# Kernel tuning notes

Measured on AMD Instinct MI355X. Metric: run time of the kernel, lower is better.

The kernel has to match this reference:

```python
import jax, jax.numpy as jnp
import numpy as np

B, S, D, H = 8, 1024, 768, 12
C = D // H  # head dim = 64
NEG_SLOPE = 0.2  # PyG GATConv default leaky_relu slope


def setup_inputs() -> dict:
    key = jax.random.key(0)
    ks = jax.random.split(key, 12)
    s = 0.02
    return {
        "hidden_states": jax.random.normal(ks[0], (B, S, D), jnp.float32),
        "transformer_output": jax.random.normal(ks[1], (B, S, D), jnp.float32),
        # GATConv params: lin (no bias), att_src/att_dst [H, C], bias [H*C]
        "W_gat": jax.random.normal(ks[2], (D, D), jnp.float32) * s,
        "att_src": jax.random.normal(ks[3], (H, C), jnp.float32) * s,
        "att_dst": jax.random.normal(ks[4], (H, C), jnp.float32) * s,
        "b_gat": jnp.zeros((D,), jnp.float32),
        # gat_projection
        "W_proj": jax.random.normal(ks[5], (D, D), jnp.float32) * s,
        "b_proj": jnp.zeros((D,), jnp.float32),
        # fusion
        "W_fus": jax.random.normal(ks[6], (2 * D, D), jnp.float32) * s,
        "b_fus": jnp.zeros((D,), jnp.float32),
    }


def reference(hidden_states, transformer_output, W_gat, att_src, att_dst,
              b_gat, W_proj, b_proj, W_fus, b_fus):
    # --- GATConv on a fully-connected graph (+ default self-loops) ---
    # Fully connected + self loops => softmax over ALL sources per target,
    # so the scatter-softmax reduces to dense attention.
    x = (hidden_states @ W_gat).reshape(B, S, H, C)          # [B,S,H,C]
    a_src = jnp.einsum('bshc,hc->bhs', x, att_src)           # score contribution of source j
    a_dst = jnp.einsum('bshc,hc->bhs', x, att_dst)           # score contribution of target i
    # scores[b,h,i,j] = a_dst_i + a_src_j, then leaky_relu, softmax over j
    scores = jax.nn.leaky_relu(a_dst[:, :, :, None] + a_src[:, :, None, :],
                               negative_slope=NEG_SLOPE)     # [B,H,S,S]
    attn = jax.nn.softmax(scores, axis=-1)
    out = jnp.einsum('bhij,bjhc->bihc', attn, x)             # aggregate sources
    gat_out = out.reshape(B, S, D) + b_gat                   # concat heads + bias

    # --- projection, fusion ---
    graph_output = gat_out @ W_proj + b_proj
    fused = jnp.concatenate([transformer_output, graph_output], axis=-1)
    fused = fused @ W_fus + b_fus
    return fused
```

## Files before the change

kernel.cpp:

```cpp
#include <hip/hip_runtime.h>
#include <hip/hip_bf16.h>

#define NB 8
#define NS 1024
#define ND 768
#define NH 12
#define NC 64
#define NEG 0.2f
#define NBUK 128

typedef __attribute__((ext_vector_type(8))) short bf16x8;
typedef __attribute__((ext_vector_type(4))) float f32x4;

static __device__ __forceinline__ float bf2f(unsigned short u) {
    union { float f; unsigned int i; } v; v.i = ((unsigned int)u) << 16; return v.f;
}
static __device__ __forceinline__ unsigned short f2bf(float f) {
    union { float f; unsigned int i; } v; v.f = f;
    unsigned int r = v.i + 0x7FFFu + ((v.i >> 16) & 1u);
    return (unsigned short)(r >> 16);
}

static __device__ __forceinline__ void gload16(const unsigned short* g, unsigned short* l) {
    __builtin_amdgcn_global_load_lds((const __attribute__((address_space(1))) void*)g,
                                     (__attribute__((address_space(3))) void*)l, 16, 0, 0);
}

static __device__ __forceinline__ int swz_bid(int orig, int nwg) {
    int q = nwg >> 3, r = nwg & 7;
    int xcd = orig & 7, idx = orig >> 3;
    return (xcd < r ? xcd * (q + 1) : r * (q + 1) + (xcd - r) * q) + idx;
}

__global__ __launch_bounds__(256) void k_prep(const float* __restrict__ hs, const float* __restrict__ to,
                                              const float* __restrict__ Wp, const float* __restrict__ Wg,
                                              const float* __restrict__ Wf, const float* __restrict__ bp,
                                              const float* __restrict__ bfu,
                                              unsigned short* __restrict__ h_bf, unsigned short* __restrict__ t_bf,
                                              unsigned short* __restrict__ Wp_bf, unsigned short* __restrict__ WgT,
                                              unsigned short* __restrict__ WfT, float* __restrict__ bias_tot,
                                              int n1, int n2) {
    const int NT1 = (ND / 32) * (3 * ND / 32);
    const int NT2 = (ND * 8) / 256;
    int blk = blockIdx.x, t = threadIdx.x;
    if (blk < NT1) {
        __shared__ float tile[32][33];
        int bx = blk % (ND / 32), by = blk / (ND / 32);
        const float* src; unsigned short* dst; int K, k0;
        if (by < ND / 32) { src = Wg; dst = WgT; K = ND; k0 = by * 32; }
        else { src = Wf; dst = WfT; K = 2 * ND; k0 = (by - ND / 32) * 32; }
        int n0 = bx * 32;
        int r = t >> 3, c4 = (t & 7) * 4;
        float4 v = *reinterpret_cast<const float4*>(src + (size_t)(k0 + r) * ND + n0 + c4);
        tile[r][c4] = v.x; tile[r][c4 + 1] = v.y; tile[r][c4 + 2] = v.z; tile[r][c4 + 3] = v.w;
        __syncthreads();
        ushort4 o;
        o.x = f2bf(tile[c4][r]); o.y = f2bf(tile[c4 + 1][r]);
        o.z = f2bf(tile[c4 + 2][r]); o.w = f2bf(tile[c4 + 3][r]);
        *reinterpret_cast<ushort4*>(dst + (size_t)(n0 + r) * K + k0 + c4) = o;
    } else if (blk < NT1 + NT2) {
        int gid = (blk - NT1) * 256 + t;
        int c = gid >> 3, sl = gid & 7;
        float acc = 0.f;
        int k0 = sl * 96;
#pragma unroll 8
        for (int k = k0; k < k0 + 96; k++) acc += bp[k] * Wf[(size_t)(ND + k) * ND + c];
        acc += __shfl_down(acc, 1, 64);
        acc += __shfl_down(acc, 2, 64);
        acc += __shfl_down(acc, 4, 64);
        if (sl == 0) bias_tot[c] = acc + bfu[c];
    } else {
        int gid = (blk - NT1 - NT2) * 256 + t;
        const float* s; unsigned short* d; int i;
        if (gid < n1) { s = hs; d = h_bf; i = gid; }
        else if (gid < 2 * n1) { s = to; d = t_bf; i = gid - n1; }
        else { s = Wp; d = Wp_bf; i = gid - 2 * n1; if (i >= n2) return; }
        i *= 4;
        float4 v = *reinterpret_cast<const float4*>(s + i);
        ushort4 o;
        o.x = f2bf(v.x); o.y = f2bf(v.y); o.z = f2bf(v.z); o.w = f2bf(v.w);
        *reinterpret_cast<ushort4*>(d + i) = o;
    }
}

__global__ __launch_bounds__(256) void k_bsumf(const unsigned short* __restrict__ x_bf,
                                               const float* __restrict__ a_src,
                                               float* __restrict__ P,
                                               float* __restrict__ zb,
                                               float* __restrict__ smax_g,
                                               float2* __restrict__ bparam) {
    int grp = blockIdx.x, bh = blockIdx.y, t = threadIdx.x;
    int b = bh / NH, h = bh % NH;
    __shared__ float v[1024];
    __shared__ float pe1[1024], pe2[1024];
    __shared__ unsigned short pj[1024];
    __shared__ float red[256];
    __shared__ int cnt[NBUK], pre[NBUK], ofs[NBUK], bst[NBUK + 1];
    __shared__ float zs1[NBUK], zs2[NBUK];
    for (int i = t; i < 1024; i += 256) v[i] = a_src[(size_t)bh * 1024 + i];
    if (t < NBUK) { cnt[t] = 0; zs1[t] = 0.f; zs2[t] = 0.f; }
    __syncthreads();
    float lm = -1e30f, ln = 1e30f;
    for (int i = t; i < 1024; i += 256) { lm = fmaxf(lm, v[i]); ln = fminf(ln, v[i]); }
    red[t] = lm; __syncthreads();
    for (int s = 128; s > 0; s >>= 1) { if (t < s) red[t] = fmaxf(red[t], red[t + s]); __syncthreads(); }
    float mx = red[0]; __syncthreads();
    red[t] = ln; __syncthreads();
    for (int s = 128; s > 0; s >>= 1) { if (t < s) red[t] = fminf(red[t], red[t + s]); __syncthreads(); }
    float mn = red[0]; __syncthreads();
    float scale = (float)NBUK / fmaxf(mx - mn, 1e-20f);
    for (int i = t; i < 1024; i += 256) {
        int bk = min(max((int)((v[i] - mn) * scale), 0), NBUK - 1);
        atomicAdd(&cnt[bk], 1);
    }
    __syncthreads();
    if (t < NBUK) pre[t] = cnt[t];
    __syncthreads();
    for (int off = 1; off < NBUK; off <<= 1) {
        int x = (t >= off && t < NBUK) ? pre[t - off] : 0;
        __syncthreads();
        if (t < NBUK) pre[t] += x;
        __syncthreads();
    }
    if (t < NBUK) {
        int start = pre[t] - cnt[t];
        bst[t] = start;
        ofs[t] = start;
    }
    if (t == 0) bst[NBUK] = 1024;
    __syncthreads();
    for (int i = t; i < 1024; i += 256) {
        int bk = min(max((int)((v[i] - mn) * scale), 0), NBUK - 1);
        float u = v[i] - mx;
        float e1 = __expf(u), e2 = __expf(0.2f * u);
        int pos = atomicAdd(&ofs[bk], 1);
        pe1[pos] = e1; pe2[pos] = e2; pj[pos] = (unsigned short)i;
        atomicAdd(&zs1[bk], e1);
        atomicAdd(&zs2[bk], e2);
    }
    __syncthreads();
    for (int off = 1; off < NBUK; off <<= 1) {
        float x1 = (t >= off && t < NBUK) ? zs1[t - off] : 0.f;
        float x2 = (t >= off && t < NBUK) ? zs2[t - off] : 0.f;
        __syncthreads();
        if (t < NBUK) { zs1[t] += x1; zs2[t] += x2; }
        __syncthreads();
    }
    if (grp == 0) {
        if (t < NBUK) {
            zb[(size_t)(bh * NBUK + t) * 2] = zs1[t];
            zb[(size_t)(bh * NBUK + t) * 2 + 1] = zs2[t];
        }
        if (t == 0) { smax_g[bh] = mx; bparam[bh] = make_float2(mn, scale); }
    }
    int w = t >> 6, lane = t & 63;
    const unsigned short* xb = x_bf + (size_t)b * NS * ND + h * 64 + lane;
#pragma unroll
    for (int r = 0; r < 2; r++) {
        int bk = grp * 8 + w * 2 + r;
        int ks = bst[bk], ke = bst[bk + 1];
        float V1 = 0.f, V2 = 0.f;
        for (int k = ks; k < ke; k++) {
            float xv = bf2f(xb[(size_t)pj[k] * ND]);
            V1 += pe1[k] * xv;
            V2 += pe2[k] * xv;
        }
        size_t o = ((size_t)(bh * NBUK + bk) * 2) * 64 + lane;
        P[o] = V1; P[o + 64] = V2;
    }
}

__global__ __launch_bounds__(256) void k_bpref(float* __restrict__ P) {
    int bh = blockIdx.x, t = threadIdx.x, w = t >> 6, lane = t & 63;
    __shared__ float segV[4][2][64];
    size_t base = (size_t)bh * NBUK;
    float V1 = 0.f, V2 = 0.f;
    for (int g = 0; g < 4; ++g) {
        float a1[8], a2[8];
#pragma unroll
        for (int r = 0; r < 8; r++) {
            size_t o = ((base + w * 32 + g * 8 + r) * 2) * 64 + lane;
            a1[r] = P[o]; a2[r] = P[o + 64];
        }
#pragma unroll
        for (int r = 0; r < 8; r++) { V1 += a1[r]; a1[r] = V1; V2 += a2[r]; a2[r] = V2; }
#pragma unroll
        for (int r = 0; r < 8; r++) {
            size_t o = ((base + w * 32 + g * 8 + r) * 2) * 64 + lane;
            P[o] = a1[r]; P[o + 64] = a2[r];
        }
    }
    segV[w][0][lane] = V1; segV[w][1][lane] = V2;
    __syncthreads();
    if (w > 0) {
        float O1 = 0.f, O2 = 0.f;
        for (int w2 = 0; w2 < w; w2++) { O1 += segV[w2][0][lane]; O2 += segV[w2][1][lane]; }
        for (int g = 0; g < 4; ++g) {
            float a1[8], a2[8];
#pragma unroll
            for (int r = 0; r < 8; r++) {
                size_t o = ((base + w * 32 + g * 8 + r) * 2) * 64 + lane;
                a1[r] = P[o]; a2[r] = P[o + 64];
            }
#pragma unroll
            for (int r = 0; r < 8; r++) {
                size_t o = ((base + w * 32 + g * 8 + r) * 2) * 64 + lane;
                P[o] = a1[r] + O1; P[o + 64] = a2[r] + O2;
            }
        }
    }
}

__global__ __launch_bounds__(256) void k_apply3(const float* __restrict__ P,
                                                const float* __restrict__ zb,
                                                const float* __restrict__ a_dst,
                                                const float* __restrict__ smax_g,
                                                const float2* __restrict__ bparam,
                                                const float* __restrict__ b_gat,
                                                unsigned short* __restrict__ gat) {
    int bh = blockIdx.y, t = threadIdx.x, w = t >> 6, lane = t & 63;
    int b = bh / NH, h = bh % NH;
    float sm = smax_g[bh];
    float2 bp_ = bparam[bh];
    float mn = bp_.x, scale = bp_.y;
    size_t pb = (size_t)bh * NBUK;
    float T1 = P[((pb + NBUK - 1) * 2) * 64 + lane];
    float z1tot = zb[(pb + NBUK - 1) * 2];
    float bias = b_gat[h * 64 + lane];
#pragma unroll
    for (int q = 0; q < 8; q++) {
        int i = blockIdx.x * 32 + w * 8 + q;
        float d = a_dst[(size_t)bh * 1024 + i];
        float dm = d + sm;
        float m = dm > 0.f ? dm : NEG * dm;
        float c1 = __expf(dm - m);
        float c2 = __expf(NEG * dm - m);
        int e = (int)floorf((-d - mn) * scale + 0.5f);
        e = min(max(e, 0), NBUK);
        float P1f = 0.f, P2f = 0.f, z1f = 0.f, z2f = 0.f;
        if (e > 0) {
            size_t o = ((pb + e - 1) * 2) * 64 + lane;
            P1f = P[o]; P2f = P[o + 64];
            z1f = zb[(pb + e - 1) * 2];
            z2f = zb[(pb + e - 1) * 2 + 1];
        }
        float num = c1 * (T1 - P1f) + c2 * P2f;
        float Z = c1 * (z1tot - z1f) + c2 * z2f;
        gat[((size_t)(b * NS + i)) * ND + h * 64 + lane] = f2bf(num / Z + bias);
    }
}

template <bool OUT_BF16, bool BIAS, bool DUAL, bool ATT>
static __device__ __forceinline__ void gemm_body(
    const unsigned short* __restrict__ A1, const unsigned short* __restrict__ B1,
    int lda1, int ldb1,
    const unsigned short* __restrict__ A2, const unsigned short* __restrict__ B2,
    int lda2, int ldb2,
    const float* __restrict__ bias, void* __restrict__ Cout,
    int m0, int n0, int N, int K,
    unsigned short* sA, unsigned short* sB,
    const float* __restrict__ att_src, const float* __restrict__ att_dst,
    float* __restrict__ a_src, float* __restrict__ a_dst) {
    int t = threadIdx.x, wave = t >> 6, lane = t & 63;
    int lr = lane & 15, kq = lane >> 4;
    int srow = t >> 3;
    int scol = ((t & 7) ^ (srow & 7)) * 8;
    int cs0 = ((kq) ^ (lr & 7)) * 8;
    int cs1 = ((4 + kq) ^ (lr & 7)) * 8;
    const int kh = K >> 6;
    const int nsteps = (DUAL ? 2 : 1) * kh;
    f32x4 acc[4][2] = {};

    auto STAGE = [&](int s, int buf) {
        const unsigned short* A; const unsigned short* Bt; int lda, ldb, k0;
        if (DUAL && s >= kh) { A = A2; Bt = B2; lda = lda2; ldb = ldb2; k0 = (s - kh) << 6; }
        else { A = A1; Bt = B1; lda = lda1; ldb = ldb1; k0 = s << 6; }
        const unsigned short* gA = A + (size_t)(m0 + srow) * lda + scol + k0;
        const unsigned short* gB = Bt + (size_t)(n0 + srow) * ldb + scol + k0;
        unsigned short* dA = sA + buf * 4096 + t * 8;
        unsigned short* dB = sB + buf * 8192 + t * 8;
        gload16(gA, dA);
        gload16(gA + (size_t)32 * lda, dA + 2048);
        gload16(gB, dB);
        gload16(gB + (size_t)32 * ldb, dB + 2048);
        gload16(gB + (size_t)64 * ldb, dB + 4096);
        gload16(gB + (size_t)96 * ldb, dB + 6144);
    };
    auto COMPUTE = [&](int cur) {
        unsigned short* cA = sA + cur * 4096;
        unsigned short* cB = sB + cur * 8192;
        bf16x8 a0[4], a1v[4], b0[2], b1v[2];
#pragma unroll
        for (int m = 0; m < 4; m++) {
            a0[m]  = *reinterpret_cast<bf16x8*>(&cA[(m * 16 + lr) * 64 + cs0]);
            a1v[m] = *reinterpret_cast<bf16x8*>(&cA[(m * 16 + lr) * 64 + cs1]);
        }
#pragma unroll
        for (int n = 0; n < 2; n++) {
            b0[n]  = *reinterpret_cast<bf16x8*>(&cB[(wave * 32 + n * 16 + lr) * 64 + cs0]);
            b1v[n] = *reinterpret_cast<bf16x8*>(&cB[(wave * 32 + n * 16 + lr) * 64 + cs1]);
        }
#pragma unroll
        for (int m = 0; m < 4; m++)
#pragma unroll
            for (int n = 0; n < 2; n++) {
                acc[m][n] = __builtin_amdgcn_mfma_f32_16x16x32_bf16(a0[m], b0[n], acc[m][n], 0, 0, 0);
                acc[m][n] = __builtin_amdgcn_mfma_f32_16x16x32_bf16(a1v[m], b1v[n], acc[m][n], 0, 0, 0);
            }
    };

    STAGE(0, 0);
    STAGE(1, 1);
    for (int s = 0; s < nsteps - 1; s++) {
        int cur = s & 1;
        asm volatile("s_waitcnt vmcnt(6)" ::: "memory");
        __builtin_amdgcn_s_barrier();
        __builtin_amdgcn_sched_barrier(0);
        COMPUTE(cur);
        __builtin_amdgcn_sched_barrier(0);
        __builtin_amdgcn_s_barrier();
        if (s + 2 < nsteps) STAGE(s + 2, cur);
    }
    asm volatile("s_waitcnt vmcnt(0)" ::: "memory");
    __builtin_amdgcn_s_barrier();
    __builtin_amdgcn_sched_barrier(0);
    COMPUTE((nsteps - 1) & 1);

    int rg = kq * 4;
#pragma unroll
    for (int m = 0; m < 4; m++) {
#pragma unroll
        for (int n = 0; n < 2; n++) {
            int col = n0 + wave * 32 + n * 16 + lr;
            float bv = BIAS ? bias[col] : 0.0f;
#pragma unroll
            for (int r = 0; r < 4; r++) {
                int row = m0 + m * 16 + rg + r;
                float v = acc[m][n][r] + bv;
                if (OUT_BF16) {
                    ((unsigned short*)Cout)[(size_t)row * N + col] = f2bf(v);
                } else {
                    ((float*)Cout)[(size_t)row * N + col] = v;
                }
            }
        }
    }

    if (ATT) {
        __syncthreads();
        float ds_[4][4] = {}, dd_[4][4] = {};
#pragma unroll
        for (int n = 0; n < 2; n++) {
            int colg = n0 + wave * 32 + n * 16 + lr;
            float as_v = att_src[colg];
            float ad_v = att_dst[colg];
#pragma unroll
            for (int m = 0; m < 4; m++)
#pragma unroll
                for (int r = 0; r < 4; r++) {
                    ds_[m][r] = fmaf(acc[m][n][r], as_v, ds_[m][r]);
                    dd_[m][r] = fmaf(acc[m][n][r], ad_v, dd_[m][r]);
                }
        }
#pragma unroll
        for (int off = 1; off <= 8; off <<= 1)
#pragma unroll
            for (int m = 0; m < 4; m++)
#pragma unroll
                for (int r = 0; r < 4; r++) {
                    ds_[m][r] += __shfl_xor(ds_[m][r], off, 64);
                    dd_[m][r] += __shfl_xor(dd_[m][r], off, 64);
                }
        float* red = (float*)sA;
        if (lr == 0) {
#pragma unroll
            for (int m = 0; m < 4; m++)
#pragma unroll
                for (int r = 0; r < 4; r++) {
                    int rl = m * 16 + kq * 4 + r;
                    red[wave * 64 + rl] = ds_[m][r];
                    red[256 + wave * 64 + rl] = dd_[m][r];
                }
        }
        __syncthreads();
        if (t < 128) {
            int hb = t >> 6, rl = t & 63;
            float vs = red[(hb * 2) * 64 + rl] + red[(hb * 2 + 1) * 64 + rl];
            float vd = red[256 + (hb * 2) * 64 + rl] + red[256 + (hb * 2 + 1) * 64 + rl];
            int grow = m0 + rl;
            int b = grow >> 10, sdx = grow & 1023;
            int head = (n0 >> 6) + hb;
            a_src[((size_t)b * NH + head) * NS + sdx] = vs;
            a_dst[((size_t)b * NH + head) * NS + sdx] = vd;
        }
    }
}

__global__ __launch_bounds__(256) void k_gemm_pair(
    const unsigned short* __restrict__ Aa, const unsigned short* __restrict__ Ba,
    unsigned short* __restrict__ Ca, int NBna, int Na, int Ka, int lda_a, int ldb_a, int nwg_a,
    const unsigned short* __restrict__ Ab, const unsigned short* __restrict__ Bb,
    unsigned short* __restrict__ Cb, int NBnb, int Nb, int Kb, int lda_b, int ldb_b,
    const float* __restrict__ att_src, const float* __restrict__ att_dst,
    float* __restrict__ a_src, float* __restrict__ a_dst) {
    __shared__ alignas(16) unsigned short sA[2 * 64 * 64];
    __shared__ alignas(16) unsigned short sB[2 * 128 * 64];
    int wg = swz_bid(blockIdx.x, gridDim.x);
    if (wg < nwg_a) {
        gemm_body<true, false, false, true>(Aa, Ba, lda_a, ldb_a, nullptr, nullptr, 0, 0, nullptr,
                                            Ca, (wg / NBna) * 64, (wg % NBna) * 128, Na, Ka, sA, sB,
                                            att_src, att_dst, a_src, a_dst);
    } else {
        wg -= nwg_a;
        gemm_body<true, false, false, false>(Ab, Bb, lda_b, ldb_b, nullptr, nullptr, 0, 0, nullptr,
                                             Cb, (wg / NBnb) * 64, (wg % NBnb) * 128, Nb, Kb, sA, sB,
                                             nullptr, nullptr, nullptr, nullptr);
    }
}

__global__ __launch_bounds__(256) void k_gemm_dual(
    const unsigned short* __restrict__ A1, const unsigned short* __restrict__ B1,
    const unsigned short* __restrict__ A2, const unsigned short* __restrict__ B2,
    const float* __restrict__ bias, float* __restrict__ out,
    int NBn, int N, int K, int lda, int ldb1, int ldb2) {
    __shared__ alignas(16) unsigned short sA[2 * 64 * 64];
    __shared__ alignas(16) unsigned short sB[2 * 128 * 64];
    int wg = swz_bid(blockIdx.x, gridDim.x);
    gemm_body<false, true, true, false>(A1, B1, lda, ldb1, A2, B2, lda, ldb2, bias,
                                        out, (wg / NBn) * 64, (wg % NBn) * 128, N, K, sA, sB,
                                        nullptr, nullptr, nullptr, nullptr);
}

extern "C" void kernel_launch(void* const* d_in, const int* in_sizes, int n_in,
                              void* d_out, int out_size, void* d_ws, size_t ws_size,
                              hipStream_t stream) {
    const float* hs  = (const float*)d_in[0];
    const float* to  = (const float*)d_in[1];
    const float* Wg  = (const float*)d_in[2];
    const float* asv = (const float*)d_in[3];
    const float* adv = (const float*)d_in[4];
    const float* bg  = (const float*)d_in[5];
    const float* Wp  = (const float*)d_in[6];
    const float* bp  = (const float*)d_in[7];
    const float* Wf  = (const float*)d_in[8];
    const float* bfu = (const float*)d_in[9];
    float* out = (float*)d_out;

    char* ws = (char*)d_ws;
    size_t off = 0;
    auto alloc = [&](size_t bytes) -> void* {
        void* p = ws + off;
        off = (off + bytes + 255) & ~(size_t)255;
        return p;
    };
    const size_t NBSD = (size_t)NB * NS * ND;
    const int NBH = NB * NH;
    unsigned short* h_bf   = (unsigned short*)alloc(NBSD * 2);
    unsigned short* x_bf   = (unsigned short*)alloc(NBSD * 2);
    unsigned short* t_bf   = (unsigned short*)alloc(NBSD * 2);
    unsigned short* WgT    = (unsigned short*)alloc((size_t)ND * ND * 2);
    unsigned short* Wp_bf  = (unsigned short*)alloc((size_t)ND * ND * 2);
    unsigned short* WfT    = (unsigned short*)alloc((size_t)2 * ND * ND * 2);
    unsigned short* WcombT = (unsigned short*)alloc((size_t)ND * ND * 2);
    float*  bias_tot = (float*)alloc((size_t)ND * 4);
    float*  a_src = (float*)alloc((size_t)NBH * NS * 4);
    float*  a_dst = (float*)alloc((size_t)NBH * NS * 4);
    float*  P     = (float*)alloc((size_t)NBH * NBUK * 2 * 64 * 4);
    float*  zb    = (float*)alloc((size_t)NBH * NBUK * 2 * 4);
    float*  smaxb = (float*)alloc((size_t)NBH * 4);
    float2* bparam = (float2*)alloc((size_t)NBH * 8);

    int n1 = (int)NBSD / 4, n2 = ND * ND / 4;
    const int NT1 = (ND / 32) * (3 * ND / 32);
    const int NT2 = (ND * 8) / 256;
    const int NT3 = (2 * n1 + n2 + 255) / 256;
    k_prep<<<NT1 + NT2 + NT3, 256, 0, stream>>>(hs, to, Wp, Wg, Wf, bp, bfu,
                                                h_bf, t_bf, Wp_bf, WgT, WfT, bias_tot, n1, n2);

    int nwg1 = (NB * NS / 64) * (ND / 128);
    int nwgW = (ND / 64) * (ND / 128);
    k_gemm_pair<<<nwg1 + nwgW, 256, 0, stream>>>(
        h_bf, WgT, x_bf, ND / 128, ND, ND, ND, ND, nwg1,
        WfT + ND, Wp_bf, WcombT, ND / 128, ND, ND, 2 * ND, ND,
        asv, adv, a_src, a_dst);

    k_bsumf<<<dim3(NBUK / 8, NBH), 256, 0, stream>>>(x_bf, a_src, P, zb, smaxb, bparam);
    k_bpref<<<NBH, 256, 0, stream>>>(P);

    unsigned short* gat_bf = h_bf;
    k_apply3<<<dim3(NS / 32, NBH), 256, 0, stream>>>(P, zb, a_dst, smaxb, bparam, bg, gat_bf);

    k_gemm_dual<<<(NB * NS / 64) * (ND / 128), 256, 0, stream>>>(
        t_bf, WfT, gat_bf, WcombT, bias_tot, out, ND / 128, ND, ND, ND, 2 * ND, ND);
}
```

Measured before the change: 136.8 us.

## Replace bucket counting-sort with LDS atomic scatter of per-bucket partial sums

The bucket-sum kernel drops the count/prefix/scatter counting sort and its serial per-bucket gather loops. Each block now owns a 16-channel slice of the head and accumulates exp-weighted x values directly into per-bucket LDS arrays with float atomics. The prefix scan of the bucket normalisers moves into k_bpref. This removes the sort barriers and the load imbalance across buckets, but adds heavy LDS atomic contention, which is worst when many sources fall into the same bucket. The grid also shrinks from 16 to 4 blocks per batch-head.

```diff
diff --git a/kernel.cpp b/kernel.cpp
--- a/kernel.cpp
+++ b/kernel.cpp
@@ -83,22 +83,23 @@
     }
 }
 
-__global__ __launch_bounds__(256) void k_bsumf(const unsigned short* __restrict__ x_bf,
-                                               const float* __restrict__ a_src,
-                                               float* __restrict__ P,
-                                               float* __restrict__ zb,
-                                               float* __restrict__ smax_g,
-                                               float2* __restrict__ bparam) {
-    int grp = blockIdx.x, bh = blockIdx.y, t = threadIdx.x;
+__global__ __launch_bounds__(256) void k_psum(const unsigned short* __restrict__ x_bf,
+                                              const float* __restrict__ a_src,
+                                              float* __restrict__ P,
+                                              float* __restrict__ zb,
+                                              float* __restrict__ smax_g,
+                                              float2* __restrict__ bparam) {
+    int cq = blockIdx.x, bh = blockIdx.y, t = threadIdx.x;
     int b = bh / NH, h = bh % NH;
+    int w = t >> 6, lane = t & 63;
+    int c = lane & 15, rr = lane >> 4;
     __shared__ float v[1024];
-    __shared__ float pe1[1024], pe2[1024];
-    __shared__ unsigned short pj[1024];
     __shared__ float red[256];
-    __shared__ int cnt[NBUK], pre[NBUK], ofs[NBUK], bst[NBUK + 1];
-    __shared__ float zs1[NBUK], zs2[NBUK];
+    __shared__ float Pl1[NBUK * 17], Pl2[NBUK * 17];
+    __shared__ float zl1[NBUK], zl2[NBUK];
     for (int i = t; i < 1024; i += 256) v[i] = a_src[(size_t)bh * 1024 + i];
-    if (t < NBUK) { cnt[t] = 0; zs1[t] = 0.f; zs2[t] = 0.f; }
+    for (int i = t; i < NBUK * 17; i += 256) { Pl1[i] = 0.f; Pl2[i] = 0.f; }
+    if (t < NBUK) { zl1[t] = 0.f; zl2[t] = 0.f; }
     __syncthreads();
     float lm = -1e30f, ln = 1e30f;
     for (int i = t; i < 1024; i += 256) { lm = fmaxf(lm, v[i]); ln = fminf(ln, v[i]); }
@@ -109,70 +110,55 @@
     for (int s = 128; s > 0; s >>= 1) { if (t < s) red[t] = fminf(red[t], red[t + s]); __syncthreads(); }
     float mn = red[0]; __syncthreads();
     float scale = (float)NBUK / fmaxf(mx - mn, 1e-20f);
-    for (int i = t; i < 1024; i += 256) {
-        int bk = min(max((int)((v[i] - mn) * scale), 0), NBUK - 1);
-        atomicAdd(&cnt[bk], 1);
+    const unsigned short* xb = x_bf + (size_t)b * NS * ND + h * 64 + cq * 16 + c;
+#pragma unroll 4
+    for (int it = 0; it < 64; it++) {
+        int j = w * 256 + it * 4 + rr;
+        float vj = v[j];
+        int bk = min(max((int)((vj - mn) * scale), 0), NBUK - 1);
+        float u = vj - mx;
+        float e1 = __expf(u), e2 = __expf(0.2f * u);
+        float xv = bf2f(xb[(size_t)j * ND]);
+        atomicAdd(&Pl1[bk * 17 + c], e1 * xv);
+        atomicAdd(&Pl2[bk * 17 + c], e2 * xv);
+        if (cq == 0 && c == 0) { atomicAdd(&zl1[bk], e1); atomicAdd(&zl2[bk], e2); }
     }
     __syncthreads();
-    if (t < NBUK) pre[t] = cnt[t];
+    for (int i = t; i < NBUK * 16; i += 256) {
+        int bk = i >> 4, cc = i & 15;
+        size_t o = ((size_t)(bh * NBUK + bk) * 2) * 64 + cq * 16 + cc;
+        P[o] = Pl1[bk * 17 + cc];
+        P[o + 64] = Pl2[bk * 17 + cc];
+    }
+    if (cq == 0) {
+        if (t < NBUK) {
+            zb[(size_t)(bh * NBUK + t) * 2] = zl1[t];
+            zb[(size_t)(bh * NBUK + t) * 2 + 1] = zl2[t];
+        }
+        if (t == 0) { smax_g[bh] = mx; bparam[bh] = make_float2(mn, scale); }
+    }
+}
+
+__global__ __launch_bounds__(256) void k_bpref(float* __restrict__ P, float* __restrict__ zb) {
+    int bh = blockIdx.x, t = threadIdx.x, w = t >> 6, lane = t & 63;
+    __shared__ float segV[4][2][64];
+    __shared__ float zsh1[NBUK], zsh2[NBUK];
+    if (t < NBUK) {
+        zsh1[t] = zb[(size_t)(bh * NBUK + t) * 2];
+        zsh2[t] = zb[(size_t)(bh * NBUK + t) * 2 + 1];
+    }
     __syncthreads();
     for (int off = 1; off < NBUK; off <<= 1) {
-        int x = (t >= off && t < NBUK) ? pre[t - off] : 0;
+        float x1 = (t >= off && t < NBUK) ? zsh1[t - off] : 0.f;
+        float x2 = (t >= off && t < NBUK) ? zsh2[t - off] : 0.f;
         __syncthreads();
-        if (t < NBUK) pre[t] += x;
+        if (t < NBUK) { zsh1[t] += x1; zsh2[t] += x2; }
         __syncthreads();
     }
     if (t < NBUK) {
-        int start = pre[t] - cnt[t];
-        bst[t] = start;
-        ofs[t] = start;
-    }
-    if (t == 0) bst[NBUK] = 1024;
-    __syncthreads();
-    for (int i = t; i < 1024; i += 256) {
-        int bk = min(max((int)((v[i] - mn) * scale), 0), NBUK - 1);
-        float u = v[i] - mx;
-        float e1 = __expf(u), e2 = __expf(0.2f * u);
-        int pos = atomicAdd(&ofs[bk], 1);
-        pe1[pos] = e1; pe2[pos] = e2; pj[pos] = (unsigned short)i;
-        atomicAdd(&zs1[bk], e1);
-        atomicAdd(&zs2[bk], e2);
-    }
-    __syncthreads();
-    for (int off = 1; off < NBUK; off <<= 1) {
-        float x1 = (t >= off && t < NBUK) ? zs1[t - off] : 0.f;
-        float x2 = (t >= off && t < NBUK) ? zs2[t - off] : 0.f;
-        __syncthreads();
-        if (t < NBUK) { zs1[t] += x1; zs2[t] += x2; }
-        __syncthreads();
-    }
-    if (grp == 0) {
-        if (t < NBUK) {
-            zb[(size_t)(bh * NBUK + t) * 2] = zs1[t];
-            zb[(size_t)(bh * NBUK + t) * 2 + 1] = zs2[t];
-        }
-        if (t == 0) { smax_g[bh] = mx; bparam[bh] = make_float2(mn, scale); }
-    }
-    int w = t >> 6, lane = t & 63;
-    const unsigned short* xb = x_bf + (size_t)b * NS * ND + h * 64 + lane;
-#pragma unroll
-    for (int r = 0; r < 2; r++) {
-        int bk = grp * 8 + w * 2 + r;
-        int ks = bst[bk], ke = bst[bk + 1];
-        float V1 = 0.f, V2 = 0.f;
-        for (int k = ks; k < ke; k++) {
-            float xv = bf2f(xb[(size_t)pj[k] * ND]);
-            V1 += pe1[k] * xv;
-            V2 += pe2[k] * xv;
-        }
-        size_t o = ((size_t)(bh * NBUK + bk) * 2) * 64 + lane;
-        P[o] = V1; P[o + 64] = V2;
-    }
-}
-
-__global__ __launch_bounds__(256) void k_bpref(float* __restrict__ P) {
-    int bh = blockIdx.x, t = threadIdx.x, w = t >> 6, lane = t & 63;
-    __shared__ float segV[4][2][64];
+        zb[(size_t)(bh * NBUK + t) * 2] = zsh1[t];
+        zb[(size_t)(bh * NBUK + t) * 2 + 1] = zsh2[t];
+    }
     size_t base = (size_t)bh * NBUK;
     float V1 = 0.f, V2 = 0.f;
     for (int g = 0; g < 4; ++g) {
@@ -484,8 +470,8 @@
         WfT + ND, Wp_bf, WcombT, ND / 128, ND, ND, 2 * ND, ND,
         asv, adv, a_src, a_dst);
 
-    k_bsumf<<<dim3(NBUK / 8, NBH), 256, 0, stream>>>(x_bf, a_src, P, zb, smaxb, bparam);
-    k_bpref<<<NBH, 256, 0, stream>>>(P);
+    k_psum<<<dim3(4, NBH), 256, 0, stream>>>(x_bf, a_src, P, zb, smaxb, bparam);
+    k_bpref<<<NBH, 256, 0, stream>>>(P, zb);
 
     unsigned short* gat_bf = h_bf;
     k_apply3<<<dim3(NS / 32, NBH), 256, 0, stream>>>(P, zb, a_dst, smaxb, bparam, bg, gat_bf);
```

Result: slower. 188.6 us (+37.9%).
